# Performance work log

Hardware: AMD Instinct MI355X
Metric: run time of the kernel (lower is better)

## Reference

```python
import jax, jax.numpy as jnp
import numpy as np

EPS = 1e-5

def _ln(x, g, b):
    mu = jnp.mean(x, axis=-1, keepdims=True)
    var = jnp.mean(jnp.square(x - mu), axis=-1, keepdims=True)
    return (x - mu) * jax.lax.rsqrt(var + EPS) * g + b


def setup_inputs() -> dict:
    key = jax.random.key(0)
    ks = jax.random.split(key, 16)
    B, T, D, H = 8, 4096, 512, 1024
    s_d = 1.0 / np.sqrt(D)
    s_h = 1.0 / np.sqrt(H)
    return {
        "x": jax.random.normal(ks[0], (B, T, D), dtype=jnp.float32),
        "gamma": jnp.ones((D,), jnp.float32),
        "beta": jnp.zeros((D,), jnp.float32),
        "Wq": jax.random.uniform(ks[1], (D, H), jnp.float32, -s_d, s_d),
        "bq": jax.random.uniform(ks[2], (H,), jnp.float32, -s_d, s_d),
        "Wk": jax.random.uniform(ks[3], (D, H), jnp.float32, -s_d, s_d),
        "bk": jax.random.uniform(ks[4], (H,), jnp.float32, -s_d, s_d),
        "Wv": jax.random.uniform(ks[5], (D, H), jnp.float32, -s_d, s_d),
        "bv": jax.random.uniform(ks[6], (H,), jnp.float32, -s_d, s_d),
        "wbias": jax.random.uniform(ks[7], (H,), jnp.float32, 0.0, 1.0),
        "Wo": jax.random.uniform(ks[8], (H, D), jnp.float32, -s_h, s_h),
        "bo": jax.random.uniform(ks[9], (D,), jnp.float32, -s_h, s_h),
        "W1": jax.random.uniform(ks[10], (D, H), jnp.float32, -s_d, s_d),
        "b1": jax.random.uniform(ks[11], (H,), jnp.float32, -s_d, s_d),
        "W2": jax.random.uniform(ks[12], (H, D), jnp.float32, -s_h, s_h),
        "b2": jax.random.uniform(ks[13], (D,), jnp.float32, -s_h, s_h),
    }


def reference(x, gamma, beta, Wq, bq, Wk, bk, Wv, bv, wbias, Wo, bo, W1, b1, W2, b2):
    # --- pre-LN ---
    x1 = _ln(x, gamma, beta)                      # [B,T,D]
    # --- AFTFull attention (NOTE: sums over BATCH dim 0, as in original repo) ---
    Q = jnp.einsum('btd,dh->bth', x1, Wq) + bq    # [B,T,H]
    K = jnp.einsum('btd,dh->bth', x1, Wk) + bk
    V = jnp.einsum('btd,dh->bth', x1, Wv) + bv
    Q_sig = jax.nn.sigmoid(Q)
    numer = jnp.exp(K + wbias)                    # [B,T,H]
    denom = jnp.sum(numer, axis=0)                # [T,H]
    weighted = jnp.sum(numer * V, axis=0) / denom # [T,H]
    Yt = Q_sig * weighted                         # [B,T,H] (broadcast)
    Yt = jnp.einsum('bth,hd->btd', Yt, Wo) + bo   # [B,T,D]
    x2 = Yt + x1                                  # residual (dropout = identity, eval)
    # --- second LN (same params, as in original) + MLP ---
    x3 = _ln(x2, gamma, beta)
    h = jax.nn.gelu(jnp.einsum('btd,dh->bth', x3, W1) + b1, approximate=False)
    m = jnp.einsum('bth,hd->btd', h, W2) + b2
    # original: out = dropout(m) + m  ==  2*m at eval (no residual to x2)
    return m + m
```

## Files before the change

kernel.cpp:

```cpp
#include <hip/hip_runtime.h>
#include <hip/hip_bf16.h>
#include <cstdint>

using u16 = unsigned short;
using u32 = unsigned int;

typedef __bf16 bf16x8 __attribute__((ext_vector_type(8)));
typedef float  f32x4  __attribute__((ext_vector_type(4)));

#define DEV static __device__ __forceinline__

DEV float bf2f(u16 u){ union { u32 u; float f; } c; c.u = ((u32)u) << 16; return c.f; }

DEV u16 f2bf(float f){
  __bf16 h = (__bf16)f;
  return __builtin_bit_cast(u16, h);
}

DEV float fast_rcp(float x){ return __builtin_amdgcn_rcpf(x); }

DEV void async16(const u16* g, u16* l){
  __builtin_amdgcn_global_load_lds((const __attribute__((address_space(1))) u32*)g,
                                   (__attribute__((address_space(3))) u32*)l,
                                   16, 0, 0);
}

__global__ __launch_bounds__(256)
void transpose_all(const float* __restrict__ W0, const float* __restrict__ W1,
                   const float* __restrict__ W2, const float* __restrict__ W3,
                   const float* __restrict__ W4, const float* __restrict__ W5,
                   u16* __restrict__ T0, u16* __restrict__ T1, u16* __restrict__ T2,
                   u16* __restrict__ T3, u16* __restrict__ T4, u16* __restrict__ T5){
  const int z = blockIdx.z;
  const float* W; u16* WT; int R, C;
  switch (z){
    case 0:  W = W0; WT = T0; R = 512;  C = 1024; break;
    case 1:  W = W1; WT = T1; R = 512;  C = 1024; break;
    case 2:  W = W2; WT = T2; R = 512;  C = 1024; break;
    case 3:  W = W3; WT = T3; R = 1024; C = 512;  break;
    case 4:  W = W4; WT = T4; R = 512;  C = 1024; break;
    default: W = W5; WT = T5; R = 1024; C = 512;  break;
  }
  const int c0 = blockIdx.x * 32, r0 = blockIdx.y * 32;
  if (c0 >= C || r0 >= R) return;
  __shared__ float tile[32][33];
  const int tx = threadIdx.x, ty = threadIdx.y;
  #pragma unroll
  for (int j = 0; j < 4; ++j)
    tile[ty + j*8][tx] = W[(size_t)(r0 + ty + j*8) * C + (c0 + tx)];
  __syncthreads();
  #pragma unroll
  for (int j = 0; j < 4; ++j)
    WT[(size_t)(c0 + ty + j*8) * R + (r0 + tx)] = f2bf(tile[tx][ty + j*8]);
}

template<bool BF16IN>
__global__ __launch_bounds__(256)
void ln_kernel(const void* __restrict__ xin, const float* __restrict__ gamma,
               const float* __restrict__ beta, u16* __restrict__ xout){
  const int wid = threadIdx.x >> 6;
  const int lane = threadIdx.x & 63;
  const size_t row = (size_t)blockIdx.x * 4 + wid;
  const int d0 = lane * 8;
  float v[8];
  if constexpr (BF16IN){
    const u16* xp = (const u16*)xin + row * 512 + d0;
    uint4 p = *(const uint4*)xp;
    const u16* s = (const u16*)&p;
    #pragma unroll
    for (int i = 0; i < 8; ++i) v[i] = bf2f(s[i]);
  } else {
    const float* xp = (const float*)xin + row * 512 + d0;
    float4 p0 = *(const float4*)xp;
    float4 p1 = *(const float4*)(xp + 4);
    v[0]=p0.x; v[1]=p0.y; v[2]=p0.z; v[3]=p0.w;
    v[4]=p1.x; v[5]=p1.y; v[6]=p1.z; v[7]=p1.w;
  }
  float s = 0.f, sq = 0.f;
  #pragma unroll
  for (int i = 0; i < 8; ++i){ s += v[i]; sq += v[i]*v[i]; }
  #pragma unroll
  for (int o = 32; o >= 1; o >>= 1){ s += __shfl_xor(s, o); sq += __shfl_xor(sq, o); }
  const float mu  = s * (1.0f/512.0f);
  const float var = sq * (1.0f/512.0f) - mu*mu;
  const float rstd = rsqrtf(var + 1e-5f);
  u16 o8[8];
  #pragma unroll
  for (int i = 0; i < 8; ++i)
    o8[i] = f2bf((v[i]-mu)*rstd*gamma[d0+i] + beta[d0+i]);
  *(uint4*)(xout + row*512 + d0) = *(const uint4*)o8;
}

__global__ __launch_bounds__(256)
void aft_weighted(const u16* __restrict__ numer, const u16* __restrict__ V,
                  u16* __restrict__ wgt){
  const size_t TH = (size_t)4096 * 1024;
  const size_t i8 = ((size_t)blockIdx.x * 256 + threadIdx.x) * 8;
  float den[8], ws[8];
  #pragma unroll
  for (int j = 0; j < 8; ++j){ den[j] = 0.f; ws[j] = 0.f; }
  #pragma unroll
  for (int b = 0; b < 8; ++b){
    uint4 pn = *(const uint4*)(numer + b*TH + i8);
    uint4 pv = *(const uint4*)(V     + b*TH + i8);
    const u16* n = (const u16*)&pn;
    const u16* v = (const u16*)&pv;
    #pragma unroll
    for (int j = 0; j < 8; ++j){ float nf = bf2f(n[j]); den[j] += nf; ws[j] += nf * bf2f(v[j]); }
  }
  u16 o[8];
  #pragma unroll
  for (int j = 0; j < 8; ++j) o[j] = f2bf(ws[j] * fast_rcp(den[j]));
  *(uint4*)(wgt + i8) = *(const uint4*)o;
}

template<int EPI, int KC, bool AMUL>
__global__ __launch_bounds__(256, 3)
void gemm128(const u16* __restrict__ A, const u16* __restrict__ Bt, int nTiles,
             const float* __restrict__ bias0, const float* __restrict__ wbias,
             u16* __restrict__ out0, u16* __restrict__ out1, u16* __restrict__ out2,
             const float* __restrict__ bias1, const float* __restrict__ bias2,
             const u16* __restrict__ resid, float* __restrict__ outf,
             const u16* __restrict__ wgt){
  __shared__ u16 ldsA[128*64];
  __shared__ u16 ldsB[128*64];
  const int tid  = threadIdx.x;
  const int wid  = tid >> 6;
  const int lane = tid & 63;
  const int quad = lane >> 4;
  const int lr   = lane & 15;

  const int lin = blockIdx.x;
  const int GS  = 16 * nTiles;
  const int g   = lin / GS;
  const int rem = lin - g * GS;
  const int tileM = (g * 16 + (rem & 15)) * 128;
  const int tileN = (rem >> 4) * 128;

  const int wmBase = (wid & 1) * 64;
  const int wnBase = (wid >> 1) * 64;

  f32x4 acc[4][4] = {};

  int srow[4], scb[4];
  #pragma unroll
  for (int r = 0; r < 4; ++r){
    const int off = r*4096 + wid*1024 + lane*16;
    srow[r] = off >> 7;
    scb[r]  = ((off >> 4) & 7) ^ (srow[r] & 7);
  }
  const u16* aSrc[4]; const u16* bSrc[4];
  const u16* wSrc[4];
  #pragma unroll
  for (int r = 0; r < 4; ++r){
    aSrc[r] = A  + (size_t)(tileM + srow[r]) * KC + scb[r]*8;
    bSrc[r] = Bt + (size_t)(tileN + srow[r]) * KC + scb[r]*8;
    if (AMUL) wSrc[r] = wgt + (size_t)((tileM + srow[r]) & 4095) * KC + scb[r]*8;
  }

  int aOff[2][4], bOff[2][4];
  #pragma unroll
  for (int s = 0; s < 2; ++s)
    #pragma unroll
    for (int i = 0; i < 4; ++i){
      const int m = wmBase + i*16 + lr;
      const int n = wnBase + i*16 + lr;
      aOff[s][i] = m*128 + (((s*4 + quad) ^ (m & 7)) * 16);
      bOff[s][i] = n*128 + (((s*4 + quad) ^ (n & 7)) * 16);
    }

  #pragma unroll
  for (int kt = 0; kt < KC; kt += 64){
    if constexpr (AMUL){
      #pragma unroll
      for (int r = 0; r < 4; ++r){
        uint4 pq = *(const uint4*)(aSrc[r] + kt);
        uint4 pw = *(const uint4*)(wSrc[r] + kt);
        const u16* q = (const u16*)&pq;
        const u16* wv = (const u16*)&pw;
        u16 o[8];
        #pragma unroll
        for (int j = 0; j < 8; ++j) o[j] = f2bf(bf2f(q[j]) * bf2f(wv[j]));
        *(uint4*)((char*)ldsA + r*4096 + wid*1024 + lane*16) = *(const uint4*)o;
      }
    } else {
      #pragma unroll
      for (int r = 0; r < 4; ++r)
        async16(aSrc[r] + kt, (u16*)((char*)ldsA + r*4096 + wid*1024));
    }
    #pragma unroll
    for (int r = 0; r < 4; ++r)
      async16(bSrc[r] + kt, (u16*)((char*)ldsB + r*4096 + wid*1024));
    __syncthreads();
    #pragma unroll
    for (int s = 0; s < 2; ++s){
      bf16x8 ar[4], br[4];
      #pragma unroll
      for (int i = 0; i < 4; ++i) ar[i] = *(const bf16x8*)((const char*)ldsA + aOff[s][i]);
      #pragma unroll
      for (int i = 0; i < 4; ++i) br[i] = *(const bf16x8*)((const char*)ldsB + bOff[s][i]);
      #pragma unroll
      for (int i = 0; i < 4; ++i)
        #pragma unroll
        for (int j = 0; j < 4; ++j)
          acc[i][j] = __builtin_amdgcn_mfma_f32_16x16x32_bf16(br[j], ar[i], acc[i][j], 0, 0, 0);
    }
    __syncthreads();
  }

  if (EPI == 0){
    const int mat = tileN >> 10;
    const float* biasP = (mat==0) ? bias0 : (mat==1) ? bias1 : bias2;
    u16* outP          = (mat==0) ? out0  : (mat==1) ? out1  : out2;
    const int h0 = (tileN & 1023) + wnBase;
    #pragma unroll
    for (int j = 0; j < 4; ++j){
      const int colb = h0 + j*16 + quad*4;
      const float4 bvv = *(const float4*)(biasP + colb);
      float4 wbv = {0,0,0,0};
      if (mat == 1) wbv = *(const float4*)(wbias + colb);
      #pragma unroll
      for (int i = 0; i < 4; ++i){
        const int row = tileM + wmBase + i*16 + lr;
        u16 o[4];
        #pragma unroll
        for (int r = 0; r < 4; ++r){
          float v = acc[i][j][r] + ((const float*)&bvv)[r];
          if (mat == 0)      v = fast_rcp(1.0f + __expf(-v));
          else if (mat == 1) v = __expf(v + ((const float*)&wbv)[r]);
          o[r] = f2bf(v);
        }
        *(uint2*)(outP + (size_t)row * 1024 + colb) = *(const uint2*)o;
      }
    }
  } else if (EPI == 1){
    #pragma unroll
    for (int j = 0; j < 4; ++j){
      const int colb = tileN + wnBase + j*16 + quad*4;
      const float4 bvv = *(const float4*)(bias0 + colb);
      #pragma unroll
      for (int i = 0; i < 4; ++i){
        const int row = tileM + wmBase + i*16 + lr;
        uint2 pr = *(const uint2*)(resid + (size_t)row * 512 + colb);
        const u16* rp = (const u16*)&pr;
        u16 o[4];
        #pragma unroll
        for (int r = 0; r < 4; ++r)
          o[r] = f2bf(acc[i][j][r] + ((const float*)&bvv)[r] + bf2f(rp[r]));
        *(uint2*)(out0 + (size_t)row * 512 + colb) = *(const uint2*)o;
      }
    }
  } else if (EPI == 2){
    #pragma unroll
    for (int j = 0; j < 4; ++j){
      const int colb = tileN + wnBase + j*16 + quad*4;
      const float4 bvv = *(const float4*)(bias0 + colb);
      #pragma unroll
      for (int i = 0; i < 4; ++i){
        const int row = tileM + wmBase + i*16 + lr;
        u16 o[4];
        #pragma unroll
        for (int r = 0; r < 4; ++r){
          float v = acc[i][j][r] + ((const float*)&bvv)[r];
          float u2 = 2.0f * v * (0.7978845608f + 0.0356774081f * v * v);
          float t  = 1.0f - 2.0f * fast_rcp(1.0f + __expf(u2));
          o[r] = f2bf(0.5f * v * (1.0f + t));
        }
        *(uint2*)(out0 + (size_t)row * 1024 + colb) = *(const uint2*)o;
      }
    }
  } else {
    #pragma unroll
    for (int j = 0; j < 4; ++j){
      const int colb = tileN + wnBase + j*16 + quad*4;
      const float4 bvv = *(const float4*)(bias0 + colb);
      #pragma unroll
      for (int i = 0; i < 4; ++i){
        const int row = tileM + wmBase + i*16 + lr;
        float4 o;
        #pragma unroll
        for (int r = 0; r < 4; ++r)
          ((float*)&o)[r] = 2.0f * (acc[i][j][r] + ((const float*)&bvv)[r]);
        *(float4*)(outf + (size_t)row * 512 + colb) = o;
      }
    }
  }
}

extern "C" void kernel_launch(void* const* d_in, const int* in_sizes, int n_in,
                              void* d_out, int out_size, void* d_ws, size_t ws_size,
                              hipStream_t stream) {
  const float* x     = (const float*)d_in[0];
  const float* gamma = (const float*)d_in[1];
  const float* beta  = (const float*)d_in[2];
  const float* Wq    = (const float*)d_in[3];
  const float* bq    = (const float*)d_in[4];
  const float* Wk    = (const float*)d_in[5];
  const float* bk    = (const float*)d_in[6];
  const float* Wv    = (const float*)d_in[7];
  const float* bv    = (const float*)d_in[8];
  const float* wbias = (const float*)d_in[9];
  const float* Wo    = (const float*)d_in[10];
  const float* bo    = (const float*)d_in[11];
  const float* W1    = (const float*)d_in[12];
  const float* b1    = (const float*)d_in[13];
  const float* W2    = (const float*)d_in[14];
  const float* b2    = (const float*)d_in[15];
  float* out = (float*)d_out;

  char* w = (char*)d_ws;
  const size_t MB = 1ull << 20;
  u16* WqkvT = (u16*)(w + 0*MB);
  u16* WoT   = (u16*)(w + 3*MB);
  u16* W1T   = (u16*)(w + 4*MB);
  u16* W2T   = (u16*)(w + 5*MB);
  u16* x1b   = (u16*)(w + 6*MB);
  u16* Qs    = (u16*)(w + 38*MB);
  u16* Nu    = (u16*)(w + 102*MB);
  u16* Vb    = (u16*)(w + 166*MB);
  u16* Wgt   = (u16*)(w + 230*MB);
  u16* x2b   = Vb;
  u16* x3b   = (u16*)(w + 198*MB);
  u16* hb    = Nu;

  transpose_all<<<dim3(32, 32, 6), dim3(32, 8), 0, stream>>>(
      Wq, Wk, Wv, Wo, W1, W2,
      WqkvT, WqkvT + 1024*512, WqkvT + 2*1024*512, WoT, W1T, W2T);

  ln_kernel<false><<<8192, 256, 0, stream>>>(x, gamma, beta, x1b);

  gemm128<0, 512, false><<<256*24, 256, 0, stream>>>(x1b, WqkvT, 24,
      bq, wbias, Qs, Nu, Vb, bk, bv, nullptr, nullptr, nullptr);

  aft_weighted<<<2048, 256, 0, stream>>>(Nu, Vb, Wgt);

  gemm128<1, 1024, true><<<256*4, 256, 0, stream>>>(Qs, WoT, 4,
      bo, nullptr, x2b, nullptr, nullptr, nullptr, nullptr, x1b, nullptr, Wgt);

  ln_kernel<true><<<8192, 256, 0, stream>>>(x2b, gamma, beta, x3b);

  gemm128<2, 512, false><<<256*8, 256, 0, stream>>>(x3b, W1T, 8,
      b1, nullptr, hb, nullptr, nullptr, nullptr, nullptr, nullptr, nullptr, nullptr);

  gemm128<3, 1024, false><<<256*4, 256, 0, stream>>>(hb, W2T, 4,
      b2, nullptr, nullptr, nullptr, nullptr, nullptr, nullptr, nullptr, out, nullptr);
}
```

Before: 513.8 us.

## Fuse Q-sigmoid multiply into AFT reduction and stage GEMM epilogue stores through LDS

The Q_sig*weighted product moves out of the Wo GEMM's A-load path into the AFT reduction kernel, which now writes a full Yt tensor. The Wo GEMM can then use async global-to-LDS loads for A instead of synchronous loads with a multiply. The bf16 GEMM epilogues are staged through LDS so each lane writes 32 contiguous bytes instead of scattered 8-byte stores. LayerNorm now loads gamma and beta as float4 vectors. The cost is an extra 64MB write and read of Yt, plus epilogue LDS traffic that reuses the A tile buffer after the final barrier.

```diff
diff --git a/kernel.cpp b/kernel.cpp
--- a/kernel.cpp
+++ b/kernel.cpp
@@ -84,16 +84,24 @@
   const float mu  = s * (1.0f/512.0f);
   const float var = sq * (1.0f/512.0f) - mu*mu;
   const float rstd = rsqrtf(var + 1e-5f);
+  const float4 g0 = *(const float4*)(gamma + d0);
+  const float4 g1 = *(const float4*)(gamma + d0 + 4);
+  const float4 b0 = *(const float4*)(beta + d0);
+  const float4 b1 = *(const float4*)(beta + d0 + 4);
+  const float* gp = (const float*)&g0;
+  float gg[8] = {g0.x,g0.y,g0.z,g0.w,g1.x,g1.y,g1.z,g1.w};
+  float bb[8] = {b0.x,b0.y,b0.z,b0.w,b1.x,b1.y,b1.z,b1.w};
+  (void)gp;
   u16 o8[8];
   #pragma unroll
   for (int i = 0; i < 8; ++i)
-    o8[i] = f2bf((v[i]-mu)*rstd*gamma[d0+i] + beta[d0+i]);
+    o8[i] = f2bf((v[i]-mu)*rstd*gg[i] + bb[i]);
   *(uint4*)(xout + row*512 + d0) = *(const uint4*)o8;
 }
 
 __global__ __launch_bounds__(256)
-void aft_weighted(const u16* __restrict__ numer, const u16* __restrict__ V,
-                  u16* __restrict__ wgt){
+void aft_fused(const u16* __restrict__ numer, const u16* __restrict__ V,
+               const u16* __restrict__ qs, u16* __restrict__ yt){
   const size_t TH = (size_t)4096 * 1024;
   const size_t i8 = ((size_t)blockIdx.x * 256 + threadIdx.x) * 8;
   float den[8], ws[8];
@@ -108,20 +116,27 @@
     #pragma unroll
     for (int j = 0; j < 8; ++j){ float nf = bf2f(n[j]); den[j] += nf; ws[j] += nf * bf2f(v[j]); }
   }
-  u16 o[8];
-  #pragma unroll
-  for (int j = 0; j < 8; ++j) o[j] = f2bf(ws[j] * fast_rcp(den[j]));
-  *(uint4*)(wgt + i8) = *(const uint4*)o;
-}
-
-template<int EPI, int KC, bool AMUL>
+  float w[8];
+  #pragma unroll
+  for (int j = 0; j < 8; ++j) w[j] = ws[j] * fast_rcp(den[j]);
+  #pragma unroll
+  for (int b = 0; b < 8; ++b){
+    uint4 pq = *(const uint4*)(qs + b*TH + i8);
+    const u16* q = (const u16*)&pq;
+    u16 o[8];
+    #pragma unroll
+    for (int j = 0; j < 8; ++j) o[j] = f2bf(bf2f(q[j]) * w[j]);
+    *(uint4*)(yt + b*TH + i8) = *(const uint4*)o;
+  }
+}
+
+template<int EPI, int KC>
 __global__ __launch_bounds__(256, 3)
 void gemm128(const u16* __restrict__ A, const u16* __restrict__ Bt, int nTiles,
              const float* __restrict__ bias0, const float* __restrict__ wbias,
              u16* __restrict__ out0, u16* __restrict__ out1, u16* __restrict__ out2,
              const float* __restrict__ bias1, const float* __restrict__ bias2,
-             const u16* __restrict__ resid, float* __restrict__ outf,
-             const u16* __restrict__ wgt){
+             const u16* __restrict__ resid, float* __restrict__ outf){
   __shared__ u16 ldsA[128*64];
   __shared__ u16 ldsB[128*64];
   const int tid  = threadIdx.x;
@@ -150,12 +165,10 @@
     scb[r]  = ((off >> 4) & 7) ^ (srow[r] & 7);
   }
   const u16* aSrc[4]; const u16* bSrc[4];
-  const u16* wSrc[4];
   #pragma unroll
   for (int r = 0; r < 4; ++r){
     aSrc[r] = A  + (size_t)(tileM + srow[r]) * KC + scb[r]*8;
     bSrc[r] = Bt + (size_t)(tileN + srow[r]) * KC + scb[r]*8;
-    if (AMUL) wSrc[r] = wgt + (size_t)((tileM + srow[r]) & 4095) * KC + scb[r]*8;
   }
 
   int aOff[2][4], bOff[2][4];
@@ -171,26 +184,11 @@
 
   #pragma unroll
   for (int kt = 0; kt < KC; kt += 64){
-    if constexpr (AMUL){
-      #pragma unroll
-      for (int r = 0; r < 4; ++r){
-        uint4 pq = *(const uint4*)(aSrc[r] + kt);
-        uint4 pw = *(const uint4*)(wSrc[r] + kt);
-        const u16* q = (const u16*)&pq;
-        const u16* wv = (const u16*)&pw;
-        u16 o[8];
-        #pragma unroll
-        for (int j = 0; j < 8; ++j) o[j] = f2bf(bf2f(q[j]) * bf2f(wv[j]));
-        *(uint4*)((char*)ldsA + r*4096 + wid*1024 + lane*16) = *(const uint4*)o;
-      }
-    } else {
-      #pragma unroll
-      for (int r = 0; r < 4; ++r)
-        async16(aSrc[r] + kt, (u16*)((char*)ldsA + r*4096 + wid*1024));
-    }
-    #pragma unroll
-    for (int r = 0; r < 4; ++r)
+    #pragma unroll
+    for (int r = 0; r < 4; ++r){
+      async16(aSrc[r] + kt, (u16*)((char*)ldsA + r*4096 + wid*1024));
       async16(bSrc[r] + kt, (u16*)((char*)ldsB + r*4096 + wid*1024));
+    }
     __syncthreads();
     #pragma unroll
     for (int s = 0; s < 2; ++s){
@@ -208,68 +206,7 @@
     __syncthreads();
   }
 
-  if (EPI == 0){
-    const int mat = tileN >> 10;
-    const float* biasP = (mat==0) ? bias0 : (mat==1) ? bias1 : bias2;
-    u16* outP          = (mat==0) ? out0  : (mat==1) ? out1  : out2;
-    const int h0 = (tileN & 1023) + wnBase;
-    #pragma unroll
-    for (int j = 0; j < 4; ++j){
-      const int colb = h0 + j*16 + quad*4;
-      const float4 bvv = *(const float4*)(biasP + colb);
-      float4 wbv = {0,0,0,0};
-      if (mat == 1) wbv = *(const float4*)(wbias + colb);
-      #pragma unroll
-      for (int i = 0; i < 4; ++i){
-        const int row = tileM + wmBase + i*16 + lr;
-        u16 o[4];
-        #pragma unroll
-        for (int r = 0; r < 4; ++r){
-          float v = acc[i][j][r] + ((const float*)&bvv)[r];
-          if (mat == 0)      v = fast_rcp(1.0f + __expf(-v));
-          else if (mat == 1) v = __expf(v + ((const float*)&wbv)[r]);
-          o[r] = f2bf(v);
-        }
-        *(uint2*)(outP + (size_t)row * 1024 + colb) = *(const uint2*)o;
-      }
-    }
-  } else if (EPI == 1){
-    #pragma unroll
-    for (int j = 0; j < 4; ++j){
-      const int colb = tileN + wnBase + j*16 + quad*4;
-      const float4 bvv = *(const float4*)(bias0 + colb);
-      #pragma unroll
-      for (int i = 0; i < 4; ++i){
-        const int row = tileM + wmBase + i*16 + lr;
-        uint2 pr = *(const uint2*)(resid + (size_t)row * 512 + colb);
-        const u16* rp = (const u16*)&pr;
-        u16 o[4];
-        #pragma unroll
-        for (int r = 0; r < 4; ++r)
-          o[r] = f2bf(acc[i][j][r] + ((const float*)&bvv)[r] + bf2f(rp[r]));
-        *(uint2*)(out0 + (size_t)row * 512 + colb) = *(const uint2*)o;
-      }
-    }
-  } else if (EPI == 2){
-    #pragma unroll
-    for (int j = 0; j < 4; ++j){
-      const int colb = tileN + wnBase + j*16 + quad*4;
-      const float4 bvv = *(const float4*)(bias0 + colb);
-      #pragma unroll
-      for (int i = 0; i < 4; ++i){
-        const int row = tileM + wmBase + i*16 + lr;
-        u16 o[4];
-        #pragma unroll
-        for (int r = 0; r < 4; ++r){
-          float v = acc[i][j][r] + ((const float*)&bvv)[r];
-          float u2 = 2.0f * v * (0.7978845608f + 0.0356774081f * v * v);
-          float t  = 1.0f - 2.0f * fast_rcp(1.0f + __expf(u2));
-          o[r] = f2bf(0.5f * v * (1.0f + t));
-        }
-        *(uint2*)(out0 + (size_t)row * 1024 + colb) = *(const uint2*)o;
-      }
-    }
-  } else {
+  if (EPI == 3){
     #pragma unroll
     for (int j = 0; j < 4; ++j){
       const int colb = tileN + wnBase + j*16 + quad*4;
@@ -284,6 +221,64 @@
         *(float4*)(outf + (size_t)row * 512 + colb) = o;
       }
     }
+    return;
+  }
+
+  u16* eb = ldsA + wid * 1152;
+  const int mat = (EPI == 0) ? (tileN >> 10) : 0;
+  const float* biasP = bias0;
+  u16* outP = out0;
+  int ldO = 1024, cb0 = tileN + wnBase;
+  if (EPI == 0){
+    biasP = (mat==0) ? bias0 : (mat==1) ? bias1 : bias2;
+    outP  = (mat==0) ? out0  : (mat==1) ? out1  : out2;
+    cb0   = (tileN & 1023) + wnBase;
+  } else if (EPI == 1){
+    ldO = 512;
+  }
+
+  #pragma unroll
+  for (int i = 0; i < 4; ++i){
+    const int row = tileM + wmBase + i*16 + lr;
+    #pragma unroll
+    for (int j = 0; j < 4; ++j){
+      const int cl = j*16 + quad*4;
+      const float4 bvv = *(const float4*)(biasP + cb0 + cl);
+      u16 o[4];
+      if (EPI == 0){
+        float4 wbv = {0,0,0,0};
+        if (mat == 1) wbv = *(const float4*)(wbias + cb0 + cl);
+        #pragma unroll
+        for (int r = 0; r < 4; ++r){
+          float v = acc[i][j][r] + ((const float*)&bvv)[r];
+          if (mat == 0)      v = fast_rcp(1.0f + __expf(-v));
+          else if (mat == 1) v = __expf(v + ((const float*)&wbv)[r]);
+          o[r] = f2bf(v);
+        }
+      } else if (EPI == 1){
+        uint2 pr = *(const uint2*)(resid + (size_t)row * 512 + cb0 + cl);
+        const u16* rp = (const u16*)&pr;
+        #pragma unroll
+        for (int r = 0; r < 4; ++r)
+          o[r] = f2bf(acc[i][j][r] + ((const float*)&bvv)[r] + bf2f(rp[r]));
+      } else {
+        #pragma unroll
+        for (int r = 0; r < 4; ++r){
+          float v = acc[i][j][r] + ((const float*)&bvv)[r];
+          float u2 = 2.0f * v * (0.7978845608f + 0.0356774081f * v * v);
+          float t  = 1.0f - 2.0f * fast_rcp(1.0f + __expf(u2));
+          o[r] = f2bf(0.5f * v * (1.0f + t));
+        }
+      }
+      *(uint2*)(eb + lr*72 + cl) = *(const uint2*)o;
+    }
+    __asm__ volatile("s_waitcnt lgkmcnt(0)" ::: "memory");
+    uint4 p0 = *(const uint4*)(eb + lr*72 + quad*16);
+    uint4 p1 = *(const uint4*)(eb + lr*72 + quad*16 + 8);
+    __asm__ volatile("s_waitcnt lgkmcnt(0)" ::: "memory");
+    u16* gp = outP + (size_t)row * ldO + cb0 + quad*16;
+    *(uint4*)gp = p0;
+    *(uint4*)(gp + 8) = p1;
   }
 }
 
@@ -318,10 +313,10 @@
   u16* Qs    = (u16*)(w + 38*MB);
   u16* Nu    = (u16*)(w + 102*MB);
   u16* Vb    = (u16*)(w + 166*MB);
-  u16* Wgt   = (u16*)(w + 230*MB);
+  u16* Yt    = Nu;
   u16* x2b   = Vb;
   u16* x3b   = (u16*)(w + 198*MB);
-  u16* hb    = Nu;
+  u16* hb    = Qs;
 
   transpose_all<<<dim3(32, 32, 6), dim3(32, 8), 0, stream>>>(
       Wq, Wk, Wv, Wo, W1, W2,
@@ -329,19 +324,19 @@
 
   ln_kernel<false><<<8192, 256, 0, stream>>>(x, gamma, beta, x1b);
 
-  gemm128<0, 512, false><<<256*24, 256, 0, stream>>>(x1b, WqkvT, 24,
-      bq, wbias, Qs, Nu, Vb, bk, bv, nullptr, nullptr, nullptr);
-
-  aft_weighted<<<2048, 256, 0, stream>>>(Nu, Vb, Wgt);
-
-  gemm128<1, 1024, true><<<256*4, 256, 0, stream>>>(Qs, WoT, 4,
-      bo, nullptr, x2b, nullptr, nullptr, nullptr, nullptr, x1b, nullptr, Wgt);
+  gemm128<0, 512><<<256*24, 256, 0, stream>>>(x1b, WqkvT, 24,
+      bq, wbias, Qs, Nu, Vb, bk, bv, nullptr, nullptr);
+
+  aft_fused<<<2048, 256, 0, stream>>>(Nu, Vb, Qs, Yt);
+
+  gemm128<1, 1024><<<256*4, 256, 0, stream>>>(Yt, WoT, 4,
+      bo, nullptr, x2b, nullptr, nullptr, nullptr, nullptr, x1b, nullptr);
 
   ln_kernel<true><<<8192, 256, 0, stream>>>(x2b, gamma, beta, x3b);
 
-  gemm128<2, 512, false><<<256*8, 256, 0, stream>>>(x3b, W1T, 8,
-      b1, nullptr, hb, nullptr, nullptr, nullptr, nullptr, nullptr, nullptr, nullptr);
-
-  gemm128<3, 1024, false><<<256*4, 256, 0, stream>>>(hb, W2T, 4,
-      b2, nullptr, nullptr, nullptr, nullptr, nullptr, nullptr, nullptr, out, nullptr);
-}
+  gemm128<2, 512><<<256*8, 256, 0, stream>>>(x3b, W1T, 8,
+      b1, nullptr, hb, nullptr, nullptr, nullptr, nullptr, nullptr, nullptr);
+
+  gemm128<3, 1024><<<256*4, 256, 0, stream>>>(hb, W2T, 4,
+      b2, nullptr, nullptr, nullptr, nullptr, nullptr, nullptr, nullptr, out);
+}
```

Measured after the change: 472.5 us. 8.0% less time.
